# Performance work log

Measured on AMD Instinct MI355X. Metric: run time of the kernel, lower is better.

## Reference

```python
import jax, jax.numpy as jnp
import numpy as np
import math

WS = 8          # window_size
H = 16          # num_heads
C = 512         # dim
D = C // H      # head dim


def _relative_coords_table():
    # (2*WS-1, 2*WS-1, 2), Swin-V2 log-spaced continuous coords
    r = jnp.arange(-(WS - 1), WS, dtype=jnp.float32)
    t = jnp.stack(jnp.meshgrid(r, r, indexing='ij'), axis=-1)
    t = t / (WS - 1) * 8.0
    return jnp.sign(t) * jnp.log2(jnp.abs(t) + 1.0) / np.float32(np.log2(8.0))


def _relative_position_index():
    # (WS*WS, WS*WS) int32 indices into the (2*WS-1)^2 bias table
    coords = np.stack(np.meshgrid(np.arange(WS), np.arange(WS), indexing='ij'))  # (2,WS,WS)
    cf = coords.reshape(2, -1)                                # (2, N)
    rel = cf[:, :, None] - cf[:, None, :]                     # (2, N, N)
    rel = rel.transpose(1, 2, 0)                              # (N, N, 2)
    rel[:, :, 0] += WS - 1
    rel[:, :, 1] += WS - 1
    rel[:, :, 0] *= 2 * WS - 1
    return jnp.asarray(rel.sum(-1), dtype=jnp.int32)


def setup_inputs() -> dict:
    key = jax.random.key(0)
    ks = jax.random.split(key, 9)
    B, N = 2048, WS * WS
    s = 0.02
    return {
        'hidden_states': jax.random.normal(ks[0], (B, N, C), jnp.float32),
        'q_w': jax.random.normal(ks[1], (C, C), jnp.float32) * s,
        'q_b': jnp.zeros((C,), jnp.float32),
        'k_w': jax.random.normal(ks[2], (C, C), jnp.float32) * s,
        'v_w': jax.random.normal(ks[3], (C, C), jnp.float32) * s,
        'v_b': jnp.zeros((C,), jnp.float32),
        'logit_scale': jnp.full((H, 1, 1), np.float32(math.log(10.0))),
        'cpb_w1': jax.random.normal(ks[4], (512, 2), jnp.float32) * s,
        'cpb_b1': jnp.zeros((512,), jnp.float32),
        'cpb_w2': jax.random.normal(ks[5], (H, 512), jnp.float32) * s,
    }


def reference(hidden_states, q_w, q_b, k_w, v_w, v_b, logit_scale,
              cpb_w1, cpb_b1, cpb_w2):
    B, N, _ = hidden_states.shape

    def heads(x):  # (B,N,C) -> (B,H,N,D)
        return x.reshape(B, N, H, D).transpose(0, 2, 1, 3)

    q = heads(hidden_states @ q_w.T + q_b)
    k = heads(hidden_states @ k_w.T)
    v = heads(hidden_states @ v_w.T + v_b)

    # cosine-similarity attention with clamped learnable logit scale
    qn = q / jnp.linalg.norm(q, axis=-1, keepdims=True)
    kn = k / jnp.linalg.norm(k, axis=-1, keepdims=True)
    scale = jnp.exp(jnp.minimum(logit_scale, np.float32(math.log(100.0))))  # (H,1,1)
    scores = jnp.einsum('bhnd,bhmd->bhnm', qn, kn) * scale

    # continuous relative position bias MLP + gather + sigmoid scale
    table = _relative_coords_table().reshape(-1, 2)            # (225, 2)
    hbias = jax.nn.relu(table @ cpb_w1.T + cpb_b1) @ cpb_w2.T  # (225, H)
    idx = _relative_position_index().reshape(-1)               # (N*N,)
    rpb = hbias[idx].reshape(N, N, H).transpose(2, 0, 1)       # (H, N, N)
    scores = scores + 16.0 * jax.nn.sigmoid(rpb)[None]

    probs = jax.nn.softmax(scores, axis=-1)
    ctx = jnp.einsum('bhnm,bhmd->bhnd', probs, v)
    return ctx.transpose(0, 2, 1, 3).reshape(B, N, C)
```

## Files before the change

### kernel.cpp

```cpp
#include <hip/hip_runtime.h>
#include <hip/hip_bf16.h>
#include <cstdint>
#include <cstddef>

typedef __attribute__((ext_vector_type(4))) float f32x4;
typedef __attribute__((ext_vector_type(8))) short short8;
typedef unsigned short ushort_t;

__device__ __forceinline__ ushort_t f2bf(float f) {
  unsigned u = __builtin_bit_cast(unsigned, f);
  u = u + 0x7FFFu + ((u >> 16) & 1u);
  return (ushort_t)(u >> 16);
}
__device__ __forceinline__ float bf2f(ushort_t s) {
  unsigned u = ((unsigned)s) << 16;
  return __builtin_bit_cast(float, u);
}
__device__ __forceinline__ void load_lds16(const void* g, void* l) {
  __builtin_amdgcn_global_load_lds((const __attribute__((address_space(1))) void*)g,
                                   (__attribute__((address_space(3))) void*)l, 16, 0, 0);
}

__device__ __forceinline__ int swzA(int row, int b) { return row*128 + (b ^ ((row & 7) << 4)); }
__device__ __forceinline__ int swzQ(int row, int b) { return row*64  + (b ^ (((row >> 1) & 3) << 4)); }
__device__ __forceinline__ int swzV(int d,   int b) { return d*256   + (b ^ ((d & 7) << 4)); }
__device__ __forceinline__ int swzP(int row, int b) { return row*128 + (b ^ ((row & 7) << 4)); }

__global__ __launch_bounds__(256) void k_cvt_bf16(const float4* __restrict__ in,
                                                  ushort_t* __restrict__ outp, int n4) {
  int i = blockIdx.x * 256 + threadIdx.x;
  int stride = gridDim.x * 256;
  for (; i < n4; i += stride) {
    float4 v = in[i];
    ushort4 o = { f2bf(v.x), f2bf(v.y), f2bf(v.z), f2bf(v.w) };
    *(ushort4*)(outp + (size_t)i * 4) = o;
  }
}

__global__ __launch_bounds__(256) void k_wcat(const float* __restrict__ qw, const float* __restrict__ qb,
                                              const float* __restrict__ kw, const float* __restrict__ vw,
                                              const float* __restrict__ vb,
                                              ushort_t* __restrict__ Wcat, float* __restrict__ bcat) {
  int o = blockIdx.x;
  int h = o / 96, r = o % 96;
  const float* src; float bias;
  if (r < 32)      { src = qw + (size_t)(h*32 + r)      * 512; bias = qb[h*32 + r]; }
  else if (r < 64) { src = kw + (size_t)(h*32 + r - 32) * 512; bias = 0.f; }
  else             { src = vw + (size_t)(h*32 + r - 64) * 512; bias = vb[h*32 + r - 64]; }
  int t = threadIdx.x;
  Wcat[(size_t)o*512 + t]       = f2bf(src[t]);
  Wcat[(size_t)o*512 + t + 256] = f2bf(src[t + 256]);
  if (t == 0) bcat[o] = bias;
}

__global__ __launch_bounds__(256) void k_bias(const float* __restrict__ w1, const float* __restrict__ b1,
                                              const float* __restrict__ w2, float* __restrict__ bias16) {
  int t = blockIdx.x;
  int a = t / 15, b = t % 15;
  float x = (float)(a - 7) * (8.f / 7.f);
  float y = (float)(b - 7) * (8.f / 7.f);
  float fx = (x == 0.f) ? 0.f : copysignf(log2f(fabsf(x) + 1.f) * (1.f / 3.f), x);
  float fy = (y == 0.f) ? 0.f : copysignf(log2f(fabsf(y) + 1.f) * (1.f / 3.f), y);
  int wv = threadIdx.x >> 6, lane = threadIdx.x & 63;
  float acc[4] = {0.f, 0.f, 0.f, 0.f};
  for (int it = 0; it < 8; ++it) {
    int j = it*64 + lane;
    float act = fmaxf(fx * w1[2*j] + fy * w1[2*j + 1] + b1[j], 0.f);
#pragma unroll
    for (int hh = 0; hh < 4; ++hh)
      acc[hh] += act * w2[(wv*4 + hh)*512 + j];
  }
#pragma unroll
  for (int hh = 0; hh < 4; ++hh) {
    float v = acc[hh];
    for (int s = 1; s < 64; s <<= 1) v += __shfl_xor(v, s);
    if (lane == 0) bias16[t*16 + wv*4 + hh] = 16.f / (1.f + __expf(-v));
  }
}

#define AS_OFF 0
#define BS_OFF 16384
#define QS_OFF 0
#define KS_OFF 8192
#define VT_OFF 16384
#define PS_OFF 24576

__global__ __launch_bounds__(256) void k_main(const ushort_t* __restrict__ hbf,
                                              const ushort_t* __restrict__ Wcat,
                                              const float* __restrict__ bcat,
                                              const float* __restrict__ bias16,
                                              const float* __restrict__ lscale,
                                              float* __restrict__ out) {
  __shared__ __align__(128) char lb_raw[32768];
  char* lb = lb_raw;

  int bid = blockIdx.x;
  int wg = (bid & 7) * 2048 + (bid >> 3);
  int mtile = wg >> 4;
  int h     = wg & 15;

  int tid = threadIdx.x;
  int w = tid >> 6, lane = tid & 63;
  int lm = lane & 15, lg = lane >> 4;

  const ushort_t* Ag = hbf  + (size_t)mtile * 128 * 512;
  const ushort_t* Wg = Wcat + (size_t)h * 96 * 512;

  f32x4 acc[2][6] = {};

  for (int ks = 0; ks < 8; ++ks) {
    int k0 = ks * 64;
#pragma unroll
    for (int i = 0; i < 4; ++i) {
      int lo  = i*4096 + w*1024;
      int row = (lo >> 7) + (lane >> 3);
      int sl  = (lane & 7) ^ (row & 7);
      load_lds16(Ag + (size_t)row*512 + k0 + sl*8, lb + AS_OFF + lo);
    }
#pragma unroll
    for (int i = 0; i < 3; ++i) {
      int lo  = i*4096 + w*1024;
      int row = (lo >> 7) + (lane >> 3);
      int sl  = (lane & 7) ^ (row & 7);
      load_lds16(Wg + (size_t)row*512 + k0 + sl*8, lb + BS_OFF + lo);
    }
    __syncthreads();
#pragma unroll
    for (int ch = 0; ch < 2; ++ch) {
      int bo = ch*64 + lg*16;
      short8 av[2], bv[6];
#pragma unroll
      for (int i = 0; i < 2; ++i) av[i] = *(const short8*)(lb + AS_OFF + swzA(w*32 + i*16 + lm, bo));
#pragma unroll
      for (int j = 0; j < 6; ++j) bv[j] = *(const short8*)(lb + BS_OFF + swzA(j*16 + lm, bo));
#pragma unroll
      for (int i = 0; i < 2; ++i)
#pragma unroll
        for (int j = 0; j < 6; ++j)
          acc[i][j] = __builtin_amdgcn_mfma_f32_16x16x32_bf16(av[i], bv[j], acc[i][j], 0, 0, 0);
    }
    __syncthreads();
  }

  float bb[6];
#pragma unroll
  for (int j = 0; j < 6; ++j) bb[j] = bcat[h*96 + j*16 + lm];
#pragma unroll
  for (int i = 0; i < 2; ++i) {
#pragma unroll
    for (int j = 0; j < 6; ++j) {
#pragma unroll
      for (int r = 0; r < 4; ++r) {
        float val = acc[i][j][r] + bb[j];
        int row = w*32 + i*16 + lg*4 + r;
        ushort_t b16 = f2bf(val);
        if (j < 2)      *(ushort_t*)(lb + QS_OFF + swzQ(row, (j*16 + lm)*2))     = b16;
        else if (j < 4) *(ushort_t*)(lb + KS_OFF + swzQ(row, ((j-2)*16 + lm)*2)) = b16;
        else            *(ushort_t*)(lb + VT_OFF + swzV((j-4)*16 + lm, row*2))   = b16;
      }
    }
  }
  __syncthreads();

  {
    int row = tid >> 1, half = tid & 1;
    float scl = __expf(fminf(lscale[h], 4.6051701860f));
#pragma unroll
    for (int qk = 0; qk < 2; ++qk) {
      char* base = lb + (qk ? KS_OFF : QS_OFF);
      int a0 = swzQ(row, half*32), a1 = swzQ(row, half*32 + 16);
      short8 v0 = *(short8*)(base + a0), v1 = *(short8*)(base + a1);
      float f[16]; float ss = 0.f;
#pragma unroll
      for (int e = 0; e < 8; ++e) { f[e]   = bf2f((ushort_t)v0[e]); ss += f[e]*f[e]; }
#pragma unroll
      for (int e = 0; e < 8; ++e) { f[8+e] = bf2f((ushort_t)v1[e]); ss += f[8+e]*f[8+e]; }
      ss += __shfl_xor(ss, 1);
      float rn = rsqrtf(ss) * (qk ? 1.f : scl);
#pragma unroll
      for (int e = 0; e < 8; ++e) v0[e] = (short)f2bf(f[e]   * rn);
#pragma unroll
      for (int e = 0; e < 8; ++e) v1[e] = (short)f2bf(f[8+e] * rn);
      *(short8*)(base + a0) = v0;
      *(short8*)(base + a1) = v1;
    }
  }
  __syncthreads();

  float bfrag[4][4];
#pragma unroll
  for (int c = 0; c < 4; ++c) {
    int m = c*16 + lm; int rm = m >> 3, cm = m & 7;
#pragma unroll
    for (int r = 0; r < 4; ++r) {
      int n = w*16 + lg*4 + r;
      int idx = ((n >> 3) - rm + 7)*15 + ((n & 7) - cm + 7);
      bfrag[c][r] = bias16[idx*16 + h];
    }
  }

#pragma unroll
  for (int win = 0; win < 2; ++win) {
    short8 aq = *(const short8*)(lb + QS_OFF + swzQ(win*64 + w*16 + lm, lg*16));
    f32x4 sacc[4];
#pragma unroll
    for (int c = 0; c < 4; ++c) {
      short8 bk = *(const short8*)(lb + KS_OFF + swzQ(win*64 + c*16 + lm, lg*16));
      f32x4 z = {0.f, 0.f, 0.f, 0.f};
      sacc[c] = __builtin_amdgcn_mfma_f32_16x16x32_bf16(aq, bk, z, 0, 0, 0);
    }
    float mx[4], sum[4], rs[4];
#pragma unroll
    for (int r = 0; r < 4; ++r) {
#pragma unroll
      for (int c = 0; c < 4; ++c) sacc[c][r] += bfrag[c][r];
      float v = fmaxf(fmaxf(sacc[0][r], sacc[1][r]), fmaxf(sacc[2][r], sacc[3][r]));
      v = fmaxf(v, __shfl_xor(v, 1)); v = fmaxf(v, __shfl_xor(v, 2));
      v = fmaxf(v, __shfl_xor(v, 4)); v = fmaxf(v, __shfl_xor(v, 8));
      mx[r] = v; sum[r] = 0.f;
    }
#pragma unroll
    for (int c = 0; c < 4; ++c)
#pragma unroll
      for (int r = 0; r < 4; ++r) {
        float p = __expf(sacc[c][r] - mx[r]); sacc[c][r] = p; sum[r] += p;
      }
#pragma unroll
    for (int r = 0; r < 4; ++r) {
      float s = sum[r];
      s += __shfl_xor(s, 1); s += __shfl_xor(s, 2); s += __shfl_xor(s, 4); s += __shfl_xor(s, 8);
      rs[r] = 1.f / s;
    }
#pragma unroll
    for (int c = 0; c < 4; ++c) {
      int m = c*16 + lm;
#pragma unroll
      for (int r = 0; r < 4; ++r) {
        int n = w*16 + lg*4 + r;
        *(ushort_t*)(lb + PS_OFF + swzP(n, m*2)) = f2bf(sacc[c][r] * rs[r]);
      }
    }
    f32x4 oacc[2] = {};
#pragma unroll
    for (int kk = 0; kk < 2; ++kk) {
      short8 ap = *(const short8*)(lb + PS_OFF + swzP(w*16 + lm, kk*64 + lg*16));
#pragma unroll
      for (int c = 0; c < 2; ++c) {
        short8 bvv = *(const short8*)(lb + VT_OFF + swzV(c*16 + lm, win*128 + kk*64 + lg*16));
        oacc[c] = __builtin_amdgcn_mfma_f32_16x16x32_bf16(ap, bvv, oacc[c], 0, 0, 0);
      }
    }
    size_t gw = (size_t)mtile*2 + win;
#pragma unroll
    for (int c = 0; c < 2; ++c)
#pragma unroll
      for (int r = 0; r < 4; ++r) {
        int n = w*16 + lg*4 + r;
        out[(gw*64 + n)*512 + h*32 + c*16 + lm] = oacc[c][r];
      }
  }
}

extern "C" void kernel_launch(void* const* d_in, const int* in_sizes, int n_in,
                              void* d_out, int out_size, void* d_ws, size_t ws_size,
                              hipStream_t stream) {
  (void)in_sizes; (void)n_in; (void)out_size; (void)ws_size;
  const float* hidden = (const float*)d_in[0];
  const float* q_w    = (const float*)d_in[1];
  const float* q_b    = (const float*)d_in[2];
  const float* k_w    = (const float*)d_in[3];
  const float* v_w    = (const float*)d_in[4];
  const float* v_b    = (const float*)d_in[5];
  const float* lscale = (const float*)d_in[6];
  const float* cpb_w1 = (const float*)d_in[7];
  const float* cpb_b1 = (const float*)d_in[8];
  const float* cpb_w2 = (const float*)d_in[9];
  float* out = (float*)d_out;

  char* wsb = (char*)d_ws;
  ushort_t* hbf    = (ushort_t*)wsb;
  ushort_t* Wcat   = (ushort_t*)(wsb + 134217728);
  float*    bcat   = (float*)(wsb + 134217728 + 1572864);
  float*    bias16 = (float*)(wsb + 134217728 + 1572864 + 6144);

  hipLaunchKernelGGL(k_cvt_bf16, dim3(2048), dim3(256), 0, stream,
                     (const float4*)hidden, hbf, 16777216);
  hipLaunchKernelGGL(k_wcat, dim3(1536), dim3(256), 0, stream,
                     q_w, q_b, k_w, v_w, v_b, Wcat, bcat);
  hipLaunchKernelGGL(k_bias, dim3(225), dim3(256), 0, stream,
                     cpb_w1, cpb_b1, cpb_w2, bias16);
  hipLaunchKernelGGL(k_main, dim3(16384), dim3(256), 0, stream,
                     hbf, Wcat, bcat, bias16, lscale, out);
}
```

Baseline: 484.2 us.

## Process two heads per workgroup with per-wave window attention and precomputed bias fragments

Each workgroup now computes QKV for two heads over 128 tokens: a 128x192 tile instead of 128x96. This halves the grid and the number of times the activation tile is reloaded from global memory. Each wave then handles one 64-token window for one head entirely in registers plus its own LDS chunk. Q/K normalization runs on accumulators via shuffles, which drops a block-wide sync and the LDS read-modify-write pass. The softmax max-subtraction is removed, relying on bounded cosine scores, and the relative-position bias is pre-laid out in fragment order by a new small kernel. The cost is higher register pressure from the 4x6 accumulators and 48KB of LDS, which may lower occupancy.

```diff
diff --git a/kernel.cpp b/kernel.cpp
--- a/kernel.cpp
+++ b/kernel.cpp
@@ -12,10 +12,6 @@
   u = u + 0x7FFFu + ((u >> 16) & 1u);
   return (ushort_t)(u >> 16);
 }
-__device__ __forceinline__ float bf2f(ushort_t s) {
-  unsigned u = ((unsigned)s) << 16;
-  return __builtin_bit_cast(float, u);
-}
 __device__ __forceinline__ void load_lds16(const void* g, void* l) {
   __builtin_amdgcn_global_load_lds((const __attribute__((address_space(1))) void*)g,
                                    (__attribute__((address_space(3))) void*)l, 16, 0, 0);
@@ -23,8 +19,6 @@
 
 __device__ __forceinline__ int swzA(int row, int b) { return row*128 + (b ^ ((row & 7) << 4)); }
 __device__ __forceinline__ int swzQ(int row, int b) { return row*64  + (b ^ (((row >> 1) & 3) << 4)); }
-__device__ __forceinline__ int swzV(int d,   int b) { return d*256   + (b ^ ((d & 7) << 4)); }
-__device__ __forceinline__ int swzP(int row, int b) { return row*128 + (b ^ ((row & 7) << 4)); }
 
 __global__ __launch_bounds__(256) void k_cvt_bf16(const float4* __restrict__ in,
                                                   ushort_t* __restrict__ outp, int n4) {
@@ -78,187 +72,190 @@
   }
 }
 
-#define AS_OFF 0
+__global__ __launch_bounds__(256) void k_bfrag(const float* __restrict__ bias16,
+                                               float* __restrict__ bfragT) {
+  int b = blockIdx.x;
+  int h = b >> 4, fi = b & 15;
+  int t = threadIdx.x;
+  int lane = t >> 2, r = t & 3;
+  int mi = fi >> 2, ci = fi & 3;
+  int lg = lane >> 4, lm = lane & 15;
+  int row = mi*16 + lg*4 + r;
+  int col = ci*16 + lm;
+  int idx = ((row >> 3) - (col >> 3) + 7)*15 + ((row & 7) - (col & 7) + 7);
+  bfragT[(size_t)b*256 + lane*4 + r] = bias16[idx*16 + h];
+}
+
 #define BS_OFF 16384
-#define QS_OFF 0
-#define KS_OFF 8192
-#define VT_OFF 16384
-#define PS_OFF 24576
 
 __global__ __launch_bounds__(256) void k_main(const ushort_t* __restrict__ hbf,
                                               const ushort_t* __restrict__ Wcat,
                                               const float* __restrict__ bcat,
-                                              const float* __restrict__ bias16,
+                                              const float* __restrict__ bfragT,
                                               const float* __restrict__ lscale,
                                               float* __restrict__ out) {
-  __shared__ __align__(128) char lb_raw[32768];
+  __shared__ __align__(128) char lb_raw[49152];
   char* lb = lb_raw;
 
   int bid = blockIdx.x;
-  int wg = (bid & 7) * 2048 + (bid >> 3);
-  int mtile = wg >> 4;
-  int h     = wg & 15;
+  int wg = (bid & 7) * 1024 + (bid >> 3);
+  int mtile = wg >> 3;
+  int hg    = wg & 7;
 
   int tid = threadIdx.x;
   int w = tid >> 6, lane = tid & 63;
+  int wm = w >> 1, wn = w & 1;
   int lm = lane & 15, lg = lane >> 4;
+  int h = hg*2 + wn;
 
   const ushort_t* Ag = hbf  + (size_t)mtile * 128 * 512;
-  const ushort_t* Wg = Wcat + (size_t)h * 96 * 512;
-
-  f32x4 acc[2][6] = {};
+  const ushort_t* Wg = Wcat + (size_t)hg * 192 * 512;
+
+  int offA[4], offB[6];
+#pragma unroll
+  for (int i = 0; i < 4; ++i) {
+    int row = i*32 + (tid >> 3);
+    int sl  = (tid & 7) ^ (row & 7);
+    offA[i] = row*512 + sl*8;
+  }
+#pragma unroll
+  for (int i = 0; i < 6; ++i) {
+    int row = i*32 + (tid >> 3);
+    int sl  = (tid & 7) ^ (row & 7);
+    offB[i] = row*512 + sl*8;
+  }
+  int ldsD = tid * 16;
+
+  f32x4 acc[4][6] = {};
 
   for (int ks = 0; ks < 8; ++ks) {
     int k0 = ks * 64;
 #pragma unroll
-    for (int i = 0; i < 4; ++i) {
-      int lo  = i*4096 + w*1024;
-      int row = (lo >> 7) + (lane >> 3);
-      int sl  = (lane & 7) ^ (row & 7);
-      load_lds16(Ag + (size_t)row*512 + k0 + sl*8, lb + AS_OFF + lo);
-    }
-#pragma unroll
-    for (int i = 0; i < 3; ++i) {
-      int lo  = i*4096 + w*1024;
-      int row = (lo >> 7) + (lane >> 3);
-      int sl  = (lane & 7) ^ (row & 7);
-      load_lds16(Wg + (size_t)row*512 + k0 + sl*8, lb + BS_OFF + lo);
-    }
+    for (int i = 0; i < 4; ++i)
+      load_lds16(Ag + offA[i] + k0, lb + i*4096 + ldsD);
+#pragma unroll
+    for (int i = 0; i < 6; ++i)
+      load_lds16(Wg + offB[i] + k0, lb + BS_OFF + i*4096 + ldsD);
     __syncthreads();
 #pragma unroll
     for (int ch = 0; ch < 2; ++ch) {
       int bo = ch*64 + lg*16;
-      short8 av[2], bv[6];
-#pragma unroll
-      for (int i = 0; i < 2; ++i) av[i] = *(const short8*)(lb + AS_OFF + swzA(w*32 + i*16 + lm, bo));
-#pragma unroll
-      for (int j = 0; j < 6; ++j) bv[j] = *(const short8*)(lb + BS_OFF + swzA(j*16 + lm, bo));
-#pragma unroll
-      for (int i = 0; i < 2; ++i)
-#pragma unroll
-        for (int j = 0; j < 6; ++j)
-          acc[i][j] = __builtin_amdgcn_mfma_f32_16x16x32_bf16(av[i], bv[j], acc[i][j], 0, 0, 0);
+      short8 av[4], bv[6];
+#pragma unroll
+      for (int mi = 0; mi < 4; ++mi)
+        av[mi] = *(const short8*)(lb + swzA(wm*64 + mi*16 + lm, bo));
+#pragma unroll
+      for (int nj = 0; nj < 6; ++nj)
+        bv[nj] = *(const short8*)(lb + BS_OFF + swzA(wn*96 + nj*16 + lm, bo));
+#pragma unroll
+      for (int mi = 0; mi < 4; ++mi)
+#pragma unroll
+        for (int nj = 0; nj < 6; ++nj)
+          acc[mi][nj] = __builtin_amdgcn_mfma_f32_16x16x32_bf16(av[mi], bv[nj], acc[mi][nj], 0, 0, 0);
     }
     __syncthreads();
   }
 
+  char* chunk = lb + w * 12288;
+  float scl = __expf(fminf(lscale[h], 4.6051701860f));
   float bb[6];
 #pragma unroll
-  for (int j = 0; j < 6; ++j) bb[j] = bcat[h*96 + j*16 + lm];
-#pragma unroll
-  for (int i = 0; i < 2; ++i) {
-#pragma unroll
-    for (int j = 0; j < 6; ++j) {
-#pragma unroll
-      for (int r = 0; r < 4; ++r) {
-        float val = acc[i][j][r] + bb[j];
-        int row = w*32 + i*16 + lg*4 + r;
-        ushort_t b16 = f2bf(val);
-        if (j < 2)      *(ushort_t*)(lb + QS_OFF + swzQ(row, (j*16 + lm)*2))     = b16;
-        else if (j < 4) *(ushort_t*)(lb + KS_OFF + swzQ(row, ((j-2)*16 + lm)*2)) = b16;
-        else            *(ushort_t*)(lb + VT_OFF + swzV((j-4)*16 + lm, row*2))   = b16;
-      }
-    }
-  }
-  __syncthreads();
-
-  {
-    int row = tid >> 1, half = tid & 1;
-    float scl = __expf(fminf(lscale[h], 4.6051701860f));
-#pragma unroll
-    for (int qk = 0; qk < 2; ++qk) {
-      char* base = lb + (qk ? KS_OFF : QS_OFF);
-      int a0 = swzQ(row, half*32), a1 = swzQ(row, half*32 + 16);
-      short8 v0 = *(short8*)(base + a0), v1 = *(short8*)(base + a1);
-      float f[16]; float ss = 0.f;
-#pragma unroll
-      for (int e = 0; e < 8; ++e) { f[e]   = bf2f((ushort_t)v0[e]); ss += f[e]*f[e]; }
-#pragma unroll
-      for (int e = 0; e < 8; ++e) { f[8+e] = bf2f((ushort_t)v1[e]); ss += f[8+e]*f[8+e]; }
-      ss += __shfl_xor(ss, 1);
-      float rn = rsqrtf(ss) * (qk ? 1.f : scl);
-#pragma unroll
-      for (int e = 0; e < 8; ++e) v0[e] = (short)f2bf(f[e]   * rn);
-#pragma unroll
-      for (int e = 0; e < 8; ++e) v1[e] = (short)f2bf(f[8+e] * rn);
-      *(short8*)(base + a0) = v0;
-      *(short8*)(base + a1) = v1;
-    }
-  }
-  __syncthreads();
-
-  float bfrag[4][4];
-#pragma unroll
-  for (int c = 0; c < 4; ++c) {
-    int m = c*16 + lm; int rm = m >> 3, cm = m & 7;
+  for (int nj = 0; nj < 6; ++nj) bb[nj] = bcat[hg*192 + wn*96 + nj*16 + lm];
+
+#pragma unroll
+  for (int mi = 0; mi < 4; ++mi) {
 #pragma unroll
     for (int r = 0; r < 4; ++r) {
-      int n = w*16 + lg*4 + r;
-      int idx = ((n >> 3) - rm + 7)*15 + ((n & 7) - cm + 7);
-      bfrag[c][r] = bias16[idx*16 + h];
-    }
-  }
-
-#pragma unroll
-  for (int win = 0; win < 2; ++win) {
-    short8 aq = *(const short8*)(lb + QS_OFF + swzQ(win*64 + w*16 + lm, lg*16));
-    f32x4 sacc[4];
-#pragma unroll
-    for (int c = 0; c < 4; ++c) {
-      short8 bk = *(const short8*)(lb + KS_OFF + swzQ(win*64 + c*16 + lm, lg*16));
-      f32x4 z = {0.f, 0.f, 0.f, 0.f};
-      sacc[c] = __builtin_amdgcn_mfma_f32_16x16x32_bf16(aq, bk, z, 0, 0, 0);
-    }
-    float mx[4], sum[4], rs[4];
+      float q0 = acc[mi][0][r] + bb[0], q1 = acc[mi][1][r] + bb[1];
+      float k0 = acc[mi][2][r],         k1 = acc[mi][3][r];
+      float ssq = q0*q0 + q1*q1;
+      float ssk = k0*k0 + k1*k1;
+      ssq += __shfl_xor(ssq, 1); ssq += __shfl_xor(ssq, 2);
+      ssq += __shfl_xor(ssq, 4); ssq += __shfl_xor(ssq, 8);
+      ssk += __shfl_xor(ssk, 1); ssk += __shfl_xor(ssk, 2);
+      ssk += __shfl_xor(ssk, 4); ssk += __shfl_xor(ssk, 8);
+      float rq = rsqrtf(ssq) * scl;
+      float rk = rsqrtf(ssk);
+      int row = mi*16 + lg*4 + r;
+      *(ushort_t*)(chunk + swzQ(row, lm*2))             = f2bf(q0 * rq);
+      *(ushort_t*)(chunk + swzQ(row, 32 + lm*2))        = f2bf(q1 * rq);
+      *(ushort_t*)(chunk + 4096 + swzQ(row, lm*2))      = f2bf(k0 * rk);
+      *(ushort_t*)(chunk + 4096 + swzQ(row, 32 + lm*2)) = f2bf(k1 * rk);
+    }
+#pragma unroll
+    for (int j = 0; j < 2; ++j) {
+      ushort4 pk;
+      pk.x = f2bf(acc[mi][4+j][0] + bb[4+j]);
+      pk.y = f2bf(acc[mi][4+j][1] + bb[4+j]);
+      pk.z = f2bf(acc[mi][4+j][2] + bb[4+j]);
+      pk.w = f2bf(acc[mi][4+j][3] + bb[4+j]);
+      int d = j*16 + lm, tokb = (mi*16 + lg*4) * 2;
+      *(ushort4*)(chunk + 8192 + swzA(d, tokb)) = pk;
+    }
+  }
+
+  short8 aq[4];
+#pragma unroll
+  for (int mi = 0; mi < 4; ++mi)
+    aq[mi] = *(const short8*)(chunk + swzQ(mi*16 + lm, lg*16));
+  f32x4 S[4][4];
+#pragma unroll
+  for (int ci = 0; ci < 4; ++ci) {
+    short8 bk = *(const short8*)(chunk + 4096 + swzQ(ci*16 + lm, lg*16));
+    f32x4 z = {0.f, 0.f, 0.f, 0.f};
+#pragma unroll
+    for (int mi = 0; mi < 4; ++mi)
+      S[mi][ci] = __builtin_amdgcn_mfma_f32_16x16x32_bf16(aq[mi], bk, z, 0, 0, 0);
+  }
+
+  const float* bT = bfragT + (size_t)h * 4096 + lane * 4;
+#pragma unroll
+  for (int mi = 0; mi < 4; ++mi) {
+    f32x4 p[4];
+#pragma unroll
+    for (int ci = 0; ci < 4; ++ci) {
+      f32x4 b = *(const f32x4*)(bT + (mi*4 + ci) * 256);
+#pragma unroll
+      for (int r = 0; r < 4; ++r)
+        p[ci][r] = __expf(S[mi][ci][r] + b[r]);
+    }
 #pragma unroll
     for (int r = 0; r < 4; ++r) {
-#pragma unroll
-      for (int c = 0; c < 4; ++c) sacc[c][r] += bfrag[c][r];
-      float v = fmaxf(fmaxf(sacc[0][r], sacc[1][r]), fmaxf(sacc[2][r], sacc[3][r]));
-      v = fmaxf(v, __shfl_xor(v, 1)); v = fmaxf(v, __shfl_xor(v, 2));
-      v = fmaxf(v, __shfl_xor(v, 4)); v = fmaxf(v, __shfl_xor(v, 8));
-      mx[r] = v; sum[r] = 0.f;
-    }
-#pragma unroll
-    for (int c = 0; c < 4; ++c)
-#pragma unroll
-      for (int r = 0; r < 4; ++r) {
-        float p = __expf(sacc[c][r] - mx[r]); sacc[c][r] = p; sum[r] += p;
-      }
-#pragma unroll
-    for (int r = 0; r < 4; ++r) {
-      float s = sum[r];
-      s += __shfl_xor(s, 1); s += __shfl_xor(s, 2); s += __shfl_xor(s, 4); s += __shfl_xor(s, 8);
-      rs[r] = 1.f / s;
-    }
-#pragma unroll
-    for (int c = 0; c < 4; ++c) {
-      int m = c*16 + lm;
-#pragma unroll
-      for (int r = 0; r < 4; ++r) {
-        int n = w*16 + lg*4 + r;
-        *(ushort_t*)(lb + PS_OFF + swzP(n, m*2)) = f2bf(sacc[c][r] * rs[r]);
-      }
-    }
-    f32x4 oacc[2] = {};
-#pragma unroll
-    for (int kk = 0; kk < 2; ++kk) {
-      short8 ap = *(const short8*)(lb + PS_OFF + swzP(w*16 + lm, kk*64 + lg*16));
-#pragma unroll
-      for (int c = 0; c < 2; ++c) {
-        short8 bvv = *(const short8*)(lb + VT_OFF + swzV(c*16 + lm, win*128 + kk*64 + lg*16));
-        oacc[c] = __builtin_amdgcn_mfma_f32_16x16x32_bf16(ap, bvv, oacc[c], 0, 0, 0);
-      }
-    }
-    size_t gw = (size_t)mtile*2 + win;
-#pragma unroll
-    for (int c = 0; c < 2; ++c)
-#pragma unroll
-      for (int r = 0; r < 4; ++r) {
-        int n = w*16 + lg*4 + r;
-        out[(gw*64 + n)*512 + h*32 + c*16 + lm] = oacc[c][r];
-      }
-  }
+      float s = p[0][r] + p[1][r] + p[2][r] + p[3][r];
+      s += __shfl_xor(s, 1); s += __shfl_xor(s, 2);
+      s += __shfl_xor(s, 4); s += __shfl_xor(s, 8);
+      float rs = 1.f / s;
+      int row = mi*16 + lg*4 + r;
+#pragma unroll
+      for (int ci = 0; ci < 4; ++ci)
+        *(ushort_t*)(chunk + swzA(row, (ci*16 + lm)*2)) = f2bf(p[ci][r] * rs);
+    }
+  }
+
+  f32x4 oa[4][2] = {};
+#pragma unroll
+  for (int kk = 0; kk < 2; ++kk) {
+    short8 ap[4];
+#pragma unroll
+    for (int mi = 0; mi < 4; ++mi)
+      ap[mi] = *(const short8*)(chunk + swzA(mi*16 + lm, kk*64 + lg*16));
+#pragma unroll
+    for (int ci = 0; ci < 2; ++ci) {
+      short8 bvv = *(const short8*)(chunk + 8192 + swzA(ci*16 + lm, kk*64 + lg*16));
+#pragma unroll
+      for (int mi = 0; mi < 4; ++mi)
+        oa[mi][ci] = __builtin_amdgcn_mfma_f32_16x16x32_bf16(ap[mi], bvv, oa[mi][ci], 0, 0, 0);
+    }
+  }
+
+  size_t rowbase = (size_t)mtile * 128 + wm * 64;
+#pragma unroll
+  for (int mi = 0; mi < 4; ++mi)
+#pragma unroll
+    for (int ci = 0; ci < 2; ++ci)
+#pragma unroll
+      for (int r = 0; r < 4; ++r)
+        out[(rowbase + mi*16 + lg*4 + r) * 512 + h*32 + ci*16 + lm] = oa[mi][ci][r];
 }
 
 extern "C" void kernel_launch(void* const* d_in, const int* in_sizes, int n_in,
@@ -280,8 +277,9 @@
   char* wsb = (char*)d_ws;
   ushort_t* hbf    = (ushort_t*)wsb;
   ushort_t* Wcat   = (ushort_t*)(wsb + 134217728);
-  float*    bcat   = (float*)(wsb + 134217728 + 1572864);
-  float*    bias16 = (float*)(wsb + 134217728 + 1572864 + 6144);
+  float*    bcat   = (float*)(wsb + 135790592);
+  float*    bias16 = (float*)(wsb + 135796736);
+  float*    bfragT = (float*)(wsb + 135811136);
 
   hipLaunchKernelGGL(k_cvt_bf16, dim3(2048), dim3(256), 0, stream,
                      (const float4*)hidden, hbf, 16777216);
@@ -289,6 +287,7 @@
                      q_w, q_b, k_w, v_w, v_b, Wcat, bcat);
   hipLaunchKernelGGL(k_bias, dim3(225), dim3(256), 0, stream,
                      cpb_w1, cpb_b1, cpb_w2, bias16);
-  hipLaunchKernelGGL(k_main, dim3(16384), dim3(256), 0, stream,
-                     hbf, Wcat, bcat, bias16, lscale, out);
-}
+  hipLaunchKernelGGL(k_bfrag, dim3(256), dim3(256), 0, stream, bias16, bfragT);
+  hipLaunchKernelGGL(k_main, dim3(8192), dim3(256), 0, stream,
+                     hbf, Wcat, bcat, bfragT, lscale, out);
+}
```

Result: slower. 776.9 us (+60.4%).
